# Performance work log

Measured on AMD Instinct MI355X. Metric: run time of the kernel, lower is better.

## Reference

```python
import jax, jax.numpy as jnp
import numpy as np

HEADS = 8
C_OUT = 256


def _gconv1x1(x, w, g):
    # x: (B, Cin, H, W); w: (Cout, Cin//g) -> grouped 1x1 conv, out (B, g, Cout//g, L)
    B, C, H, W = x.shape
    xr = x.reshape(B, g, C // g, H * W)
    wr = w.reshape(g, w.shape[0] // g, C // g)
    return jnp.einsum('god,bgdl->bgol', wr, xr)


def _sine_pe(d, L, dtype):
    # standard transformer sinusoidal PE laid out as (channels=d, positions=L)
    pos = jnp.arange(L, dtype=jnp.float32)
    i = jnp.arange(0, d, 2, dtype=jnp.float32)
    inv_freq = jnp.exp(-np.float32(np.log(10000.0)) * i / d)  # (d/2,)
    ang = inv_freq[:, None] * pos[None, :]                    # (d/2, L)
    pe = jnp.zeros((d, L), jnp.float32)
    pe = pe.at[0::2].set(jnp.sin(ang)).at[1::2].set(jnp.cos(ang))
    return pe.astype(dtype)


def setup_inputs() -> dict:
    key = jax.random.key(0)
    k1, k2, k3, k4 = jax.random.split(key, 4)
    B, Cin, H, W = 2, 256, 24, 24
    std = np.float32(np.sqrt(2.0 / C_OUT))  # kaiming_normal fan_out, relu gain
    x = jax.random.normal(k1, (B, Cin, H, W), jnp.float32)
    wq = jax.random.normal(k2, (C_OUT, Cin // HEADS), jnp.float32) * std
    wk = jax.random.normal(k3, (C_OUT, Cin // HEADS), jnp.float32) * std
    wv = jax.random.normal(k4, (C_OUT, Cin // HEADS), jnp.float32) * std
    return {"x": x, "wq": wq, "wk": wk, "wv": wv}


def reference(x, wq, wk, wv):
    B, Cin, H, W = x.shape
    g = HEADS
    d = C_OUT // g
    L = H * W
    q = _gconv1x1(x, wq, g)  # (B, g, d, L)
    k = _gconv1x1(x, wk, g)
    v = _gconv1x1(x, wv, g)
    # sinusoidal positional encoding added to keys over flattened spatial dim
    pe = _sine_pe(C_OUT, L, x.dtype)
    k = (k.reshape(B, C_OUT, L) + pe[None]).reshape(B, g, d, L)
    # NOTE: original torch code flattens batch AND heads into the attention dim
    qf = q.transpose(0, 1, 3, 2).reshape(-1, d)   # (N, d), N = B*g*L
    kf = k.transpose(2, 0, 1, 3).reshape(d, -1)   # (d, N)
    vf = v.transpose(0, 1, 3, 2).reshape(-1, d)   # (N, d)
    scale = np.float32(np.sqrt(g / C_OUT))        # = 1/sqrt(d)
    att = jax.nn.softmax(qf @ kf * scale, axis=-1)  # (N, N)
    out = att @ vf                                  # (N, d)
    out = out.reshape(B, g, L, d).transpose(0, 1, 3, 2).reshape(B, C_OUT, H, W)
    return out
```

## Files before the change

kernel.cpp:

```cpp
#include <hip/hip_runtime.h>


#define LSP   576
#define NROW  9216
#define DH    32
#define SPLIT 8
#define KPB   (NROW / SPLIT)
#define BN    64
#define NTILE (KPB / BN)
#define KSTR  40
#define VSTR  72
#define PSTR  72

typedef __attribute__((ext_vector_type(8))) short bh8;
typedef __attribute__((ext_vector_type(4))) float f4;

static __device__ __forceinline__ float bf2f(unsigned short u) {
    union { unsigned int i; float f; } w; w.i = (unsigned int)u << 16; return w.f;
}
static __device__ __forceinline__ unsigned short f2bf(float x) {
    union { float f; unsigned int i; } w; w.f = x;
    unsigned int u = w.i;
    return (unsigned short)((u + 0x7fffu + ((u >> 16) & 1u)) >> 16);
}
static __device__ __forceinline__ unsigned int pkbf(float a, float b) {
    return (unsigned int)f2bf(a) | ((unsigned int)f2bf(b) << 16);
}

__global__ __launch_bounds__(256) void sa_proj_kernel(
    const float* __restrict__ x,
    const float* __restrict__ wq, const float* __restrict__ wk, const float* __restrict__ wv,
    unsigned short* __restrict__ Qhi, unsigned short* __restrict__ Qlo,
    unsigned short* __restrict__ Khi, unsigned short* __restrict__ Vhi)
{
    __shared__ __align__(16) float xs[32 * 40];
    __shared__ float vt[32 * 37];
    __shared__ float wqs[32 * 33], wks[32 * 33], wvs[32 * 33];
    const int t = threadIdx.x;
    const int bg = blockIdx.x >> 4;
    const int part = blockIdx.x & 15;
    const int g = bg & 7;
    const int l0 = part * 36;

    const float* xp = x + (size_t)bg * 32 * LSP + l0;
    for (int i = t; i < 32 * 9; i += 256) {
        int d = i / 9, seg = i % 9;
        *(float4*)(xs + d * 40 + seg * 4) = *(const float4*)(xp + d * LSP + seg * 4);
    }
    for (int i = t; i < 1024; i += 256) {
        int o = i >> 5, d = i & 31;
        wqs[o * 33 + d] = wq[(g * 32 + o) * 32 + d];
        wks[o * 33 + d] = wk[(g * 32 + o) * 32 + d];
        wvs[o * 33 + d] = wv[(g * 32 + o) * 32 + d];
    }
    __syncthreads();

    const float scale = 0.17677669529663687f;
    for (int idx = t; idx < 32 * 36; idx += 256) {
        const int o = idx & 31;
        const int lloc = idx >> 5;
        const int l = l0 + lloc;
        float aq = 0.f, ak = 0.f, av = 0.f;
        #pragma unroll
        for (int d = 0; d < 32; d++) {
            const float xv = xs[d * 40 + lloc];
            aq = fmaf(wqs[o * 33 + d], xv, aq);
            ak = fmaf(wks[o * 33 + d], xv, ak);
            av = fmaf(wvs[o * 33 + d], xv, av);
        }
        aq *= scale;
        const int c = g * 32 + o;
        const float i2 = (float)(c & ~1);
        const float inv = __expf(-0.035977892078031968f * i2);
        float sv, cv;
        __sincosf(inv * (float)l, &sv, &cv);
        ak += (c & 1) ? cv : sv;

        const size_t row = (size_t)bg * LSP + l;
        const unsigned short h = f2bf(aq);
        Qhi[row * 32 + o] = h;
        Qlo[row * 32 + o] = f2bf(aq - bf2f(h));
        Khi[row * 32 + o] = f2bf(ak);
        vt[o * 37 + lloc] = av;
    }
    __syncthreads();

    for (int idx = t; idx < 32 * 36; idx += 256) {
        const int d = idx / 36;
        const int cc = idx - d * 36;
        Vhi[(size_t)d * NROW + (size_t)bg * LSP + l0 + cc] = f2bf(vt[d * 37 + cc]);
    }
}

__global__ __launch_bounds__(256, 4) void sa_attn_kernel(
    const unsigned short* __restrict__ Qhi, const unsigned short* __restrict__ Qlo,
    const unsigned short* __restrict__ Khi, const unsigned short* __restrict__ Vhi,
    float* __restrict__ PACC)
{
    __shared__ __align__(16) unsigned short khi_s[BN * KSTR];
    __shared__ __align__(16) unsigned short vhi_s[DH * VSTR];
    __shared__ __align__(16) unsigned short ps[4 * 32 * PSTR];

    const int t = threadIdx.x;
    const int wave = t >> 6, lane = t & 63;
    const int quad = lane >> 4, l16 = lane & 15;
    const int n0w = blockIdx.x * 128 + wave * 32;
    const int sp = blockIdx.y;

    const bh8 qh0 = *(const bh8*)(Qhi + (size_t)(n0w + l16) * DH + quad * 8);
    const bh8 ql0 = *(const bh8*)(Qlo + (size_t)(n0w + l16) * DH + quad * 8);
    const bh8 qh1 = *(const bh8*)(Qhi + (size_t)(n0w + 16 + l16) * DH + quad * 8);
    const bh8 ql1 = *(const bh8*)(Qlo + (size_t)(n0w + 16 + l16) * DH + quad * 8);

    unsigned short* psw = ps + wave * 32 * PSTR;

    f4 o00 = {0.f,0.f,0.f,0.f}, o01 = {0.f,0.f,0.f,0.f};
    f4 o10 = {0.f,0.f,0.f,0.f}, o11 = {0.f,0.f,0.f,0.f};
    float ls0 = 0.f, ls1 = 0.f;
    const f4 zf = {0.f,0.f,0.f,0.f};

    const int kr = t >> 2, ksg = t & 3;
    const int vr = t >> 3, vsg = t & 7;
    const int k0 = sp * KPB;

    uint4 kreg = *(const uint4*)(Khi + (size_t)(k0 + kr) * DH + ksg * 8);
    uint4 vreg = *(const uint4*)(Vhi + (size_t)vr * NROW + k0 + vsg * 8);

    for (int tile = 0; tile < NTILE; tile++) {
        __syncthreads();
        *(uint4*)(khi_s + kr * KSTR + ksg * 8) = kreg;
        *(uint4*)(vhi_s + vr * VSTR + vsg * 8) = vreg;
        __syncthreads();
        if (tile + 1 < NTILE) {
            const int kn = k0 + (tile + 1) * BN;
            kreg = *(const uint4*)(Khi + (size_t)(kn + kr) * DH + ksg * 8);
            vreg = *(const uint4*)(Vhi + (size_t)vr * NROW + kn + vsg * 8);
        }

        #pragma unroll
        for (int jj = 0; jj < 4; jj++) {
            const bh8 kh = *(const bh8*)(khi_s + (jj * 16 + l16) * KSTR + quad * 8);
            f4 s0 = __builtin_amdgcn_mfma_f32_16x16x32_bf16(kh, ql0, zf, 0, 0, 0);
            s0 = __builtin_amdgcn_mfma_f32_16x16x32_bf16(kh, qh0, s0, 0, 0, 0);
            f4 s1 = __builtin_amdgcn_mfma_f32_16x16x32_bf16(kh, ql1, zf, 0, 0, 0);
            s1 = __builtin_amdgcn_mfma_f32_16x16x32_bf16(kh, qh1, s1, 0, 0, 0);

            float e0 = __expf(s0[0]), e1 = __expf(s0[1]),
                  e2 = __expf(s0[2]), e3 = __expf(s0[3]);
            ls0 += (e0 + e1) + (e2 + e3);
            uint2 pk0; pk0.x = pkbf(e0, e1); pk0.y = pkbf(e2, e3);
            *(uint2*)(psw + l16 * PSTR + jj * 16 + quad * 4) = pk0;

            e0 = __expf(s1[0]); e1 = __expf(s1[1]);
            e2 = __expf(s1[2]); e3 = __expf(s1[3]);
            ls1 += (e0 + e1) + (e2 + e3);
            uint2 pk1; pk1.x = pkbf(e0, e1); pk1.y = pkbf(e2, e3);
            *(uint2*)(psw + (16 + l16) * PSTR + jj * 16 + quad * 4) = pk1;
        }

        #pragma unroll
        for (int kk = 0; kk < 2; kk++) {
            const bh8 pa0 = *(const bh8*)(psw + l16 * PSTR + kk * 32 + quad * 8);
            const bh8 pa1 = *(const bh8*)(psw + (16 + l16) * PSTR + kk * 32 + quad * 8);
            const bh8 v0  = *(const bh8*)(vhi_s + l16 * VSTR + kk * 32 + quad * 8);
            const bh8 v1  = *(const bh8*)(vhi_s + (16 + l16) * VSTR + kk * 32 + quad * 8);
            o00 = __builtin_amdgcn_mfma_f32_16x16x32_bf16(pa0, v0, o00, 0, 0, 0);
            o01 = __builtin_amdgcn_mfma_f32_16x16x32_bf16(pa0, v1, o01, 0, 0, 0);
            o10 = __builtin_amdgcn_mfma_f32_16x16x32_bf16(pa1, v0, o10, 0, 0, 0);
            o11 = __builtin_amdgcn_mfma_f32_16x16x32_bf16(pa1, v1, o11, 0, 0, 0);
        }
    }

    ls0 += __shfl_xor(ls0, 16); ls0 += __shfl_xor(ls0, 32);
    ls1 += __shfl_xor(ls1, 16); ls1 += __shfl_xor(ls1, 32);

    #pragma unroll
    for (int reg = 0; reg < 4; reg++) {
        const int q0 = n0w + quad * 4 + reg;
        float* p0 = PACC + ((size_t)q0 * SPLIT + sp) * 36;
        p0[l16]      = o00[reg];
        p0[16 + l16] = o01[reg];
        float* p1 = PACC + ((size_t)(q0 + 16) * SPLIT + sp) * 36;
        p1[l16]      = o10[reg];
        p1[16 + l16] = o11[reg];
    }
    if (quad == 0) {
        PACC[((size_t)(n0w + l16) * SPLIT + sp) * 36 + 32]      = ls0;
        PACC[((size_t)(n0w + 16 + l16) * SPLIT + sp) * 36 + 32] = ls1;
    }
}

__global__ __launch_bounds__(256) void sa_merge_kernel(
    const float* __restrict__ PACC, float* __restrict__ out)
{
    const int gid = blockIdx.x * 256 + threadIdx.x;
    const int n = gid >> 5;
    const int dch = gid & 31;
    const float* base = PACC + (size_t)n * SPLIT * 36;
    float num = 0.f, den = 0.f;
    #pragma unroll
    for (int s = 0; s < SPLIT; s++) {
        num += base[s * 36 + dch];
        den += base[s * 36 + 32];
    }
    const int bg = n / LSP;
    const int l = n - bg * LSP;
    out[((size_t)bg * 32 + dch) * LSP + l] = num / den;
}

extern "C" void kernel_launch(void* const* d_in, const int* in_sizes, int n_in,
                              void* d_out, int out_size, void* d_ws, size_t ws_size,
                              hipStream_t stream) {
    (void)in_sizes; (void)n_in; (void)out_size; (void)ws_size;
    const float* x  = (const float*)d_in[0];
    const float* wq = (const float*)d_in[1];
    const float* wk = (const float*)d_in[2];
    const float* wv = (const float*)d_in[3];

    unsigned short* ws = (unsigned short*)d_ws;
    const size_t SZ = (size_t)NROW * DH;
    unsigned short* Qhi = ws;
    unsigned short* Qlo = ws + SZ;
    unsigned short* Khi = ws + 2 * SZ;
    unsigned short* Vhi = ws + 3 * SZ;
    float* PACC = (float*)(ws + 4 * SZ);
    float* out = (float*)d_out;

    sa_proj_kernel<<<256, 256, 0, stream>>>(x, wq, wk, wv, Qhi, Qlo, Khi, Vhi);
    sa_attn_kernel<<<dim3(72, SPLIT), 256, 0, stream>>>(Qhi, Qlo, Khi, Vhi, PACC);
    sa_merge_kernel<<<NROW * DH / 256, 256, 0, stream>>>(PACC, out);
}
```

Measured before the change: 109.2 us.

## Split keys across waves within a block and merge partials in shared memory

The attention kernel now gives each block 36 queries and splits the key range across 8 waves. Each wave reads K fragments straight from global memory into registers and V from a tile-blocked transposed layout, so the block-wide K/V shared-memory staging and its barriers are gone. Partial outputs and row sums are reduced in shared memory at the end of the block, which removes the separate merge kernel and the global partial-accumulator round trip. The cost is redundant MFMA work on padded query rows (48 computed for 36 used), more registers per wave, and only 256 blocks to spread across the GPU.

```diff
diff --git a/kernel.cpp b/kernel.cpp
--- a/kernel.cpp
+++ b/kernel.cpp
@@ -4,13 +4,15 @@
 #define LSP   576
 #define NROW  9216
 #define DH    32
-#define SPLIT 8
-#define KPB   (NROW / SPLIT)
-#define BN    64
-#define NTILE (KPB / BN)
-#define KSTR  40
-#define VSTR  72
-#define PSTR  72
+#define NW    8
+#define KPW   (NROW / NW)
+#define BN    32
+#define NTILE (KPW / BN)
+#define VSTR  40
+#define PSTR  40
+#define QB    36
+#define SZ    ((size_t)NROW * DH)
+#define SZP   (SZ + 2048)
 
 typedef __attribute__((ext_vector_type(8))) short bh8;
 typedef __attribute__((ext_vector_type(4))) float f4;
@@ -27,11 +29,13 @@
     return (unsigned int)f2bf(a) | ((unsigned int)f2bf(b) << 16);
 }
 
+#define MFMA(a, b, c) __builtin_amdgcn_mfma_f32_16x16x32_bf16(a, b, c, 0, 0, 0)
+
 __global__ __launch_bounds__(256) void sa_proj_kernel(
     const float* __restrict__ x,
     const float* __restrict__ wq, const float* __restrict__ wk, const float* __restrict__ wv,
     unsigned short* __restrict__ Qhi, unsigned short* __restrict__ Qlo,
-    unsigned short* __restrict__ Khi, unsigned short* __restrict__ Vhi)
+    unsigned short* __restrict__ Khi, unsigned short* __restrict__ Vt)
 {
     __shared__ __align__(16) float xs[32 * 40];
     __shared__ float vt[32 * 37];
@@ -88,124 +92,125 @@
     for (int idx = t; idx < 32 * 36; idx += 256) {
         const int d = idx / 36;
         const int cc = idx - d * 36;
-        Vhi[(size_t)d * NROW + (size_t)bg * LSP + l0 + cc] = f2bf(vt[d * 37 + cc]);
-    }
-}
-
-__global__ __launch_bounds__(256, 4) void sa_attn_kernel(
+        const int n = bg * LSP + l0 + cc;
+        Vt[(size_t)(n >> 5) * 1024 + d * 32 + (n & 31)] = f2bf(vt[d * 37 + cc]);
+    }
+}
+
+__global__ __launch_bounds__(512, 2) void sa_attn_kernel(
     const unsigned short* __restrict__ Qhi, const unsigned short* __restrict__ Qlo,
-    const unsigned short* __restrict__ Khi, const unsigned short* __restrict__ Vhi,
-    float* __restrict__ PACC)
+    const unsigned short* __restrict__ Khi, const unsigned short* __restrict__ Vt,
+    float* __restrict__ out)
 {
-    __shared__ __align__(16) unsigned short khi_s[BN * KSTR];
-    __shared__ __align__(16) unsigned short vhi_s[DH * VSTR];
-    __shared__ __align__(16) unsigned short ps[4 * 32 * PSTR];
-
+    __shared__ __align__(16) unsigned short shm[NW * 3200];
     const int t = threadIdx.x;
     const int wave = t >> 6, lane = t & 63;
     const int quad = lane >> 4, l16 = lane & 15;
-    const int n0w = blockIdx.x * 128 + wave * 32;
-    const int sp = blockIdx.y;
-
-    const bh8 qh0 = *(const bh8*)(Qhi + (size_t)(n0w + l16) * DH + quad * 8);
-    const bh8 ql0 = *(const bh8*)(Qlo + (size_t)(n0w + l16) * DH + quad * 8);
-    const bh8 qh1 = *(const bh8*)(Qhi + (size_t)(n0w + 16 + l16) * DH + quad * 8);
-    const bh8 ql1 = *(const bh8*)(Qlo + (size_t)(n0w + 16 + l16) * DH + quad * 8);
-
-    unsigned short* psw = ps + wave * 32 * PSTR;
+    const int n0 = blockIdx.x * QB;
+
+    unsigned short* vs = shm + wave * 3200;
+    unsigned short* ps = vs + 32 * VSTR;
+
+    const bh8 qh0 = *(const bh8*)(Qhi + (size_t)(n0 + l16) * DH + quad * 8);
+    const bh8 ql0 = *(const bh8*)(Qlo + (size_t)(n0 + l16) * DH + quad * 8);
+    const bh8 qh1 = *(const bh8*)(Qhi + (size_t)(n0 + 16 + l16) * DH + quad * 8);
+    const bh8 ql1 = *(const bh8*)(Qlo + (size_t)(n0 + 16 + l16) * DH + quad * 8);
+    const bh8 qh2 = *(const bh8*)(Qhi + (size_t)(n0 + 32 + l16) * DH + quad * 8);
+    const bh8 ql2 = *(const bh8*)(Qlo + (size_t)(n0 + 32 + l16) * DH + quad * 8);
 
     f4 o00 = {0.f,0.f,0.f,0.f}, o01 = {0.f,0.f,0.f,0.f};
     f4 o10 = {0.f,0.f,0.f,0.f}, o11 = {0.f,0.f,0.f,0.f};
-    float ls0 = 0.f, ls1 = 0.f;
+    f4 o20 = {0.f,0.f,0.f,0.f}, o21 = {0.f,0.f,0.f,0.f};
+    float ls0 = 0.f, ls1 = 0.f, ls2 = 0.f;
     const f4 zf = {0.f,0.f,0.f,0.f};
 
-    const int kr = t >> 2, ksg = t & 3;
-    const int vr = t >> 3, vsg = t & 7;
-    const int k0 = sp * KPB;
-
-    uint4 kreg = *(const uint4*)(Khi + (size_t)(k0 + kr) * DH + ksg * 8);
-    uint4 vreg = *(const uint4*)(Vhi + (size_t)vr * NROW + k0 + vsg * 8);
-
-    for (int tile = 0; tile < NTILE; tile++) {
-        __syncthreads();
-        *(uint4*)(khi_s + kr * KSTR + ksg * 8) = kreg;
-        *(uint4*)(vhi_s + vr * VSTR + vsg * 8) = vreg;
-        __syncthreads();
+    const int kbase = wave * KPW;
+    bh8 kf0 = *(const bh8*)(Khi + (size_t)(kbase + l16) * DH + quad * 8);
+    bh8 kf1 = *(const bh8*)(Khi + (size_t)(kbase + 16 + l16) * DH + quad * 8);
+    uint4 va = *(const uint4*)(Vt + (size_t)(kbase >> 5) * 1024 + lane * 8);
+    uint4 vb = *(const uint4*)(Vt + (size_t)(kbase >> 5) * 1024 + 512 + lane * 8);
+
+    for (int tile = 0; tile < NTILE; ++tile) {
+        *(uint4*)(vs + (lane >> 2) * VSTR + (lane & 3) * 8) = va;
+        *(uint4*)(vs + (16 + (lane >> 2)) * VSTR + (lane & 3) * 8) = vb;
+
+        f4 s00 = MFMA(kf0, ql0, zf); s00 = MFMA(kf0, qh0, s00);
+        f4 s01 = MFMA(kf0, ql1, zf); s01 = MFMA(kf0, qh1, s01);
+        f4 s02 = MFMA(kf0, ql2, zf); s02 = MFMA(kf0, qh2, s02);
+        f4 s10 = MFMA(kf1, ql0, zf); s10 = MFMA(kf1, qh0, s10);
+        f4 s11 = MFMA(kf1, ql1, zf); s11 = MFMA(kf1, qh1, s11);
+        f4 s12 = MFMA(kf1, ql2, zf); s12 = MFMA(kf1, qh2, s12);
+
         if (tile + 1 < NTILE) {
-            const int kn = k0 + (tile + 1) * BN;
-            kreg = *(const uint4*)(Khi + (size_t)(kn + kr) * DH + ksg * 8);
-            vreg = *(const uint4*)(Vhi + (size_t)vr * NROW + kn + vsg * 8);
-        }
-
-        #pragma unroll
-        for (int jj = 0; jj < 4; jj++) {
-            const bh8 kh = *(const bh8*)(khi_s + (jj * 16 + l16) * KSTR + quad * 8);
-            f4 s0 = __builtin_amdgcn_mfma_f32_16x16x32_bf16(kh, ql0, zf, 0, 0, 0);
-            s0 = __builtin_amdgcn_mfma_f32_16x16x32_bf16(kh, qh0, s0, 0, 0, 0);
-            f4 s1 = __builtin_amdgcn_mfma_f32_16x16x32_bf16(kh, ql1, zf, 0, 0, 0);
-            s1 = __builtin_amdgcn_mfma_f32_16x16x32_bf16(kh, qh1, s1, 0, 0, 0);
-
-            float e0 = __expf(s0[0]), e1 = __expf(s0[1]),
-                  e2 = __expf(s0[2]), e3 = __expf(s0[3]);
-            ls0 += (e0 + e1) + (e2 + e3);
-            uint2 pk0; pk0.x = pkbf(e0, e1); pk0.y = pkbf(e2, e3);
-            *(uint2*)(psw + l16 * PSTR + jj * 16 + quad * 4) = pk0;
-
-            e0 = __expf(s1[0]); e1 = __expf(s1[1]);
-            e2 = __expf(s1[2]); e3 = __expf(s1[3]);
-            ls1 += (e0 + e1) + (e2 + e3);
-            uint2 pk1; pk1.x = pkbf(e0, e1); pk1.y = pkbf(e2, e3);
-            *(uint2*)(psw + (16 + l16) * PSTR + jj * 16 + quad * 4) = pk1;
-        }
-
-        #pragma unroll
-        for (int kk = 0; kk < 2; kk++) {
-            const bh8 pa0 = *(const bh8*)(psw + l16 * PSTR + kk * 32 + quad * 8);
-            const bh8 pa1 = *(const bh8*)(psw + (16 + l16) * PSTR + kk * 32 + quad * 8);
-            const bh8 v0  = *(const bh8*)(vhi_s + l16 * VSTR + kk * 32 + quad * 8);
-            const bh8 v1  = *(const bh8*)(vhi_s + (16 + l16) * VSTR + kk * 32 + quad * 8);
-            o00 = __builtin_amdgcn_mfma_f32_16x16x32_bf16(pa0, v0, o00, 0, 0, 0);
-            o01 = __builtin_amdgcn_mfma_f32_16x16x32_bf16(pa0, v1, o01, 0, 0, 0);
-            o10 = __builtin_amdgcn_mfma_f32_16x16x32_bf16(pa1, v0, o10, 0, 0, 0);
-            o11 = __builtin_amdgcn_mfma_f32_16x16x32_bf16(pa1, v1, o11, 0, 0, 0);
-        }
+            const int kn = kbase + (tile + 1) * BN;
+            kf0 = *(const bh8*)(Khi + (size_t)(kn + l16) * DH + quad * 8);
+            kf1 = *(const bh8*)(Khi + (size_t)(kn + 16 + l16) * DH + quad * 8);
+            va = *(const uint4*)(Vt + (size_t)(kn >> 5) * 1024 + lane * 8);
+            vb = *(const uint4*)(Vt + (size_t)(kn >> 5) * 1024 + 512 + lane * 8);
+        }
+
+        #define EXPST(S, GRP, JJ, LSV)                                        \
+        {                                                                     \
+            const float e0 = __expf(S[0]), e1 = __expf(S[1]);                 \
+            const float e2 = __expf(S[2]), e3 = __expf(S[3]);                 \
+            LSV += (e0 + e1) + (e2 + e3);                                     \
+            uint2 pk; pk.x = pkbf(e0, e1); pk.y = pkbf(e2, e3);               \
+            *(uint2*)(ps + (GRP * 16 + l16) * PSTR + JJ * 16 + quad * 4) = pk;\
+        }
+        EXPST(s00, 0, 0, ls0) EXPST(s01, 1, 0, ls1) EXPST(s02, 2, 0, ls2)
+        EXPST(s10, 0, 1, ls0) EXPST(s11, 1, 1, ls1) EXPST(s12, 2, 1, ls2)
+        #undef EXPST
+
+        const bh8 pa0 = *(const bh8*)(ps + l16 * PSTR + quad * 8);
+        const bh8 pa1 = *(const bh8*)(ps + (16 + l16) * PSTR + quad * 8);
+        const bh8 pa2 = *(const bh8*)(ps + (32 + l16) * PSTR + quad * 8);
+        const bh8 v0  = *(const bh8*)(vs + l16 * VSTR + quad * 8);
+        const bh8 v1  = *(const bh8*)(vs + (16 + l16) * VSTR + quad * 8);
+        o00 = MFMA(pa0, v0, o00); o01 = MFMA(pa0, v1, o01);
+        o10 = MFMA(pa1, v0, o10); o11 = MFMA(pa1, v1, o11);
+        o20 = MFMA(pa2, v0, o20); o21 = MFMA(pa2, v1, o21);
     }
 
     ls0 += __shfl_xor(ls0, 16); ls0 += __shfl_xor(ls0, 32);
     ls1 += __shfl_xor(ls1, 16); ls1 += __shfl_xor(ls1, 32);
-
+    ls2 += __shfl_xor(ls2, 16); ls2 += __shfl_xor(ls2, 32);
+
+    __syncthreads();
+    float* mo = (float*)shm;
+    float* mls = mo + NW * 1160;
+    float* mp = mo + wave * 1160;
     #pragma unroll
-    for (int reg = 0; reg < 4; reg++) {
-        const int q0 = n0w + quad * 4 + reg;
-        float* p0 = PACC + ((size_t)q0 * SPLIT + sp) * 36;
-        p0[l16]      = o00[reg];
-        p0[16 + l16] = o01[reg];
-        float* p1 = PACC + ((size_t)(q0 + 16) * SPLIT + sp) * 36;
-        p1[l16]      = o10[reg];
-        p1[16 + l16] = o11[reg];
+    for (int reg = 0; reg < 4; ++reg) {
+        const int q0 = quad * 4 + reg;
+        mp[l16 * 36 + q0]             = o00[reg];
+        mp[(16 + l16) * 36 + q0]      = o01[reg];
+        mp[l16 * 36 + 16 + q0]        = o10[reg];
+        mp[(16 + l16) * 36 + 16 + q0] = o11[reg];
+        if (quad == 0) {
+            mp[l16 * 36 + 32 + reg]        = o20[reg];
+            mp[(16 + l16) * 36 + 32 + reg] = o21[reg];
+        }
     }
     if (quad == 0) {
-        PACC[((size_t)(n0w + l16) * SPLIT + sp) * 36 + 32]      = ls0;
-        PACC[((size_t)(n0w + 16 + l16) * SPLIT + sp) * 36 + 32] = ls1;
-    }
-}
-
-__global__ __launch_bounds__(256) void sa_merge_kernel(
-    const float* __restrict__ PACC, float* __restrict__ out)
-{
-    const int gid = blockIdx.x * 256 + threadIdx.x;
-    const int n = gid >> 5;
-    const int dch = gid & 31;
-    const float* base = PACC + (size_t)n * SPLIT * 36;
-    float num = 0.f, den = 0.f;
-    #pragma unroll
-    for (int s = 0; s < SPLIT; s++) {
-        num += base[s * 36 + dch];
-        den += base[s * 36 + 32];
-    }
-    const int bg = n / LSP;
-    const int l = n - bg * LSP;
-    out[((size_t)bg * 32 + dch) * LSP + l] = num / den;
+        mls[wave * 36 + l16]      = ls0;
+        mls[wave * 36 + 16 + l16] = ls1;
+        if (l16 < 4) mls[wave * 36 + 32 + l16] = ls2;
+    }
+    __syncthreads();
+
+    const int bg = n0 / LSP;
+    const int l0 = n0 - bg * LSP;
+    for (int c = t; c < 32 * QB; c += 512) {
+        const int d = c / QB;
+        const int q = c - d * QB;
+        float num = 0.f, den = 0.f;
+        #pragma unroll
+        for (int w2 = 0; w2 < NW; ++w2) {
+            num += mo[w2 * 1160 + c];
+            den += mls[w2 * 36 + q];
+        }
+        out[((size_t)(bg * 32 + d)) * LSP + l0 + q] = num / den;
+    }
 }
 
 extern "C" void kernel_launch(void* const* d_in, const int* in_sizes, int n_in,
@@ -218,15 +223,12 @@
     const float* wv = (const float*)d_in[3];
 
     unsigned short* ws = (unsigned short*)d_ws;
-    const size_t SZ = (size_t)NROW * DH;
     unsigned short* Qhi = ws;
-    unsigned short* Qlo = ws + SZ;
-    unsigned short* Khi = ws + 2 * SZ;
-    unsigned short* Vhi = ws + 3 * SZ;
-    float* PACC = (float*)(ws + 4 * SZ);
+    unsigned short* Qlo = ws + SZP;
+    unsigned short* Khi = ws + 2 * SZP;
+    unsigned short* Vt  = ws + 3 * SZP;
     float* out = (float*)d_out;
 
-    sa_proj_kernel<<<256, 256, 0, stream>>>(x, wq, wk, wv, Qhi, Qlo, Khi, Vhi);
-    sa_attn_kernel<<<dim3(72, SPLIT), 256, 0, stream>>>(Qhi, Qlo, Khi, Vhi, PACC);
-    sa_merge_kernel<<<NROW * DH / 256, 256, 0, stream>>>(PACC, out);
-}
+    sa_proj_kernel<<<256, 256, 0, stream>>>(x, wq, wk, wv, Qhi, Qlo, Khi, Vt);
+    sa_attn_kernel<<<256, 512, 0, stream>>>(Qhi, Qlo, Khi, Vt, out);
+}
```

After: 102.2 us. -6.4%, faster.
